# Performance work log

Hardware: AMD Instinct MI355X
Metric: run time of the kernel (lower is better)

## Reference

```python
import jax, jax.numpy as jnp
import numpy as np

VOCAB = 128
NUM_PATHS = 100     # num_paths sampled from the lattice
NBEST_SCALE = 0.5   # scale on scores before sampling (k2.random_paths)
TEMPERATURE = 1.0   # logprob temperature before normalization
BLANK = 0           # CTC blank token


def setup_inputs() -> dict:
    key = jax.random.key(0)
    k1, k2, k3, k4 = jax.random.split(key, 4)
    B, T, L = 8, 500, 100
    logits = jax.random.normal(k1, (B, T, VOCAB), jnp.float32)
    emissions = jax.nn.log_softmax(logits, -1)  # acoustic-model log-probs (N, T, C)
    emissions_lengths = jax.random.randint(k2, (B,), 400, T + 1).astype(jnp.int32)
    labels = jax.random.randint(k3, (B, L), 1, VOCAB).astype(jnp.int32)
    labels_length = jax.random.randint(k4, (B,), 80, L + 1).astype(jnp.int32)
    return {"emissions": emissions, "emissions_lengths": emissions_lengths,
            "labels": labels, "labels_length": labels_length}


def _mwer(emissions, emissions_lengths, labels, labels_length):
    B, T, V = emissions.shape
    L = labels.shape[1]
    P = NUM_PATHS
    key = jax.random.key(1)
    # --- N-best path sampling: Gumbel perturbation of nbest_scale-scaled log-probs ---
    u = jax.random.uniform(key, (B, P, T, V), emissions.dtype, 1e-6, 1.0 - 1e-6)
    g = -jnp.log(-jnp.log(u))
    tokens = jnp.argmax(emissions[:, None] * NBEST_SCALE + g, axis=-1)  # (B, P, T)
    frame_mask = jnp.arange(T)[None, None, :] < emissions_lengths[:, None, None]
    # path log-prob under the model (unscaled scores), temperature-scaled
    lp = jnp.take_along_axis(emissions[:, None], tokens[..., None], axis=-1)[..., 0]
    path_logp = jnp.sum(jnp.where(frame_mask, lp, 0.0), axis=-1) / TEMPERATURE  # (B, P)
    # --- CTC collapse (ctc_topo semantics: drop blanks + repeats) into padded hyps ---
    prev = jnp.concatenate([jnp.full_like(tokens[..., :1], -1), tokens[..., :-1]], -1)
    keep = (tokens != BLANK) & (tokens != prev) & frame_mask
    pos = jnp.where(keep, jnp.cumsum(keep, -1) - 1, T)  # dropped frames -> dump slot T
    BP = B * P
    tok2, pos2 = tokens.reshape(BP, T), pos.reshape(BP, T)
    hyp = jnp.full((BP, T + 1), -1, tokens.dtype).at[jnp.arange(BP)[:, None], pos2].set(tok2)[:, :T]
    hyp_len = keep.reshape(BP, T).sum(-1)
    # --- Levenshtein alignment: exact edit distance hyp vs ref (vectorized DP) ---
    refs = jnp.repeat(labels, P, axis=0)             # (BP, L)  hyp_to_ref_map
    ref_len = jnp.repeat(labels_length, P, axis=0)   # (BP,)
    dp0 = jnp.broadcast_to(jnp.arange(L + 1, dtype=jnp.int32), (BP, L + 1))
    js = jnp.arange(L + 1, dtype=jnp.int32)[None, :]

    def step(dp, x):
        h, valid = x  # hyp token (BP,), valid flag (BP,)
        cost = (refs != h[:, None]).astype(jnp.int32)                       # (BP, L)
        cand = jnp.concatenate([dp[:, :1] + 1,
                                jnp.minimum(dp[:, 1:] + 1, dp[:, :-1] + cost)], 1)
        # insertion chain new[j] = min(cand[j], new[j-1]+1) via min-plus prefix
        new = jax.lax.cummin(cand - js, axis=1) + js
        return jnp.where(valid[:, None], new, dp), None

    valid = jnp.arange(T)[:, None] < hyp_len[None, :]  # (T, BP)
    dp, _ = jax.lax.scan(step, dp0, (hyp.T, valid))
    wers = jnp.take_along_axis(dp, ref_len[:, None], 1)[:, 0].reshape(B, P)
    wers = jax.lax.stop_gradient(wers.astype(emissions.dtype))
    # --- MWER: normalize path posteriors per utterance, expected WER, 'mean' ---
    prob = jax.nn.softmax(path_logp, axis=1)
    return jnp.mean(prob * wers)


def reference(emissions, emissions_lengths, labels, labels_length):
    return _mwer(emissions, emissions_lengths, labels, labels_length)
```

## Files before the change

kernel.cpp:

```cpp
#include <hip/hip_runtime.h>
#include <stdint.h>

#define NB 8
#define NP 100
#define NT 500
#define NV 128
#define NBP 800
#define TS 512
#define NITEMS (NB * NT * 50)
#define ROWD 129

typedef unsigned long long u64;

#define ROTL(x, r) __builtin_amdgcn_alignbit((x), (x), 32 - (r))

__device__ __forceinline__ uint32_t threefry01_lo(uint32_t x0, uint32_t x1) {
  const uint32_t k0 = 0u, k1 = 1u;
  const uint32_t k2 = 0x1BD11BDAu ^ k0 ^ k1;
  x0 += k0; x1 += k1;
#define TF_R(r) { x0 += x1; x1 = ROTL(x1, r); x1 ^= x0; }
  TF_R(13) TF_R(15) TF_R(26) TF_R(6)
  x0 += k1; x1 += k2 + 1u;
  TF_R(17) TF_R(29) TF_R(16) TF_R(24)
  x0 += k2; x1 += k0 + 2u;
  TF_R(13) TF_R(15) TF_R(26) TF_R(6)
  x0 += k0; x1 += k1 + 3u;
  TF_R(17) TF_R(29) TF_R(16) TF_R(24)
  x0 += k1; x1 += k2 + 4u;
  TF_R(13) TF_R(15) TF_R(26) TF_R(6)
  x1 += k0 + 5u;
#undef TF_R
  return x1;
}

__global__ __launch_bounds__(256) void k_sample(
    const float* __restrict__ em, const int* __restrict__ elen,
    uint8_t* __restrict__ tok2, float* __restrict__ lp2) {
  __shared__ float snw[4][NV + 1];
  const int tid = threadIdx.x;
  const int item0 = blockIdx.x * 128;
  const int R0 = item0 / 50;
  for (int i = tid; i < 4 * NV; i += 256) {
    const int r = i >> 7, v = i & 127;
    int R = R0 + r; R = R < NB * NT ? R : NB * NT - 1;
    snw[r][v] = -__builtin_amdgcn_exp2f(em[(size_t)R * NV + v] * -0.7213475204444817f);
  }
  __syncthreads();
  const int gg = blockIdx.x * 256 + tid;
  const int item = gg >> 1, half = gg & 1;
  if (item >= NITEMS) return;
  const int R = item / 50;
  const int pp = item - R * 50;
  const int b = R / NT;
  const int t = R - b * NT;
  if (t >= elen[b]) return;
  const int r = R - R0;
  const int vh = half << 6;
  const int bp0 = b * NP + 2 * pp;
  const uint32_t base0 = ((uint32_t)(bp0 * NT + t) << 7) + (uint32_t)vh;
  const uint32_t base1 = base0 + (uint32_t)(NT << 7);
  const float span = (float)(1.0 - 1e-6) - 1e-6f;
  float best0 = 3.0e38f, best1 = 3.0e38f;
  int bi0 = 0, bi1 = 0;
#pragma unroll 8
  for (int i = 0; i < 64; i++) {
    const uint32_t r0 = threefry01_lo(0u, base0 + (uint32_t)i);
    const uint32_t r1 = threefry01_lo(0u, base1 + (uint32_t)i);
    const float f0 = __uint_as_float((r0 >> 9) | 0x3f800000u) - 1.0f;
    const float f1 = __uint_as_float((r1 >> 9) | 0x3f800000u) - 1.0f;
    const float u0 = fmaf(f0, span, 1e-6f);
    const float u1 = fmaf(f1, span, 1e-6f);
    const float w = snw[r][vh + i];
    const float s0 = __log2f(u0) * w;
    const float s1 = __log2f(u1) * w;
    if (s0 < best0) { best0 = s0; bi0 = vh + i; }
    if (s1 < best1) { best1 = s1; bi1 = vh + i; }
  }
  {
    const float ob = __shfl_xor(best0, 1); const int oi = __shfl_xor(bi0, 1);
    if (ob < best0 || (ob == best0 && oi < bi0)) { best0 = ob; bi0 = oi; }
    const float ob1 = __shfl_xor(best1, 1); const int oi1 = __shfl_xor(bi1, 1);
    if (ob1 < best1 || (ob1 == best1 && oi1 < bi1)) { best1 = ob1; bi1 = oi1; }
  }
  if (half == 0) {
    const float e0 = em[(size_t)R * NV + bi0];
    const float e1 = em[(size_t)R * NV + bi1];
    tok2[(size_t)bp0 * TS + t] = (uint8_t)bi0;
    tok2[(size_t)(bp0 + 1) * TS + t] = (uint8_t)bi1;
    lp2[(size_t)bp0 * TS + t] = e0;
    lp2[(size_t)(bp0 + 1) * TS + t] = e1;
  }
}

struct Eq4 { u64 e0[4], e1[4]; int cc[4]; };

__device__ __forceinline__ void ext4(uint32_t wbits, const uint32_t* __restrict__ pqf,
                                     Eq4& E) {
#pragma unroll
  for (int i = 0; i < 4; i++) {
    const int byte = (wbits >> (8 * i)) & 255;
    const int c = byte & 127;
    E.cc[i] = byte;
    E.e0[i] = (u64)pqf[c] | ((u64)pqf[128 + c] << 32);
    E.e1[i] = (u64)pqf[256 + c] | ((u64)pqf[384 + c] << 32);
  }
}

__device__ __forceinline__ void proc4(const Eq4& E, int fbase, int myel,
                                      int hw, u64 hmask,
                                      u64& Pv0, u64& Pv1, u64& Mv0, u64& Mv1,
                                      int& score, int& prev) {
#pragma unroll
  for (int i = 0; i < 4; i++) {
    if (fbase + i >= myel) break;
    const int c = E.cc[i];
    const bool kept = (c != 0) && (c != prev);
    prev = c;
    if (kept) {
      const u64 Eq0 = E.e0[i], Eq1 = E.e1[i];
      const u64 Xv0 = Eq0 | Mv0, Xv1 = Eq1 | Mv1;
      const u64 EP0 = Eq0 & Pv0, EP1 = Eq1 & Pv1;
      const u64 sA = EP0 + Pv0;
      const u64 sB = EP1 + Pv1 + (sA < EP0 ? 1ull : 0ull);
      const u64 Xh0 = (sA ^ Pv0) | Eq0;
      const u64 Xh1 = (sB ^ Pv1) | Eq1;
      const u64 Ph0 = Mv0 | ~(Xh0 | Pv0);
      const u64 Ph1 = Mv1 | ~(Xh1 | Pv1);
      const u64 Mh0 = Pv0 & Xh0, Mh1 = Pv1 & Xh1;
      score += (int)(((hw ? Ph1 : Ph0) & hmask) != 0);
      score -= (int)(((hw ? Mh1 : Mh0) & hmask) != 0);
      const u64 nPh1 = (Ph1 << 1) | (Ph0 >> 63);
      const u64 nPh0 = (Ph0 << 1) | 1ull;
      const u64 nMh1 = (Mh1 << 1) | (Mh0 >> 63);
      const u64 nMh0 = (Mh0 << 1);
      Pv0 = nMh0 | ~(Xv0 | nPh0);
      Pv1 = nMh1 | ~(Xv1 | nPh1);
      Mv0 = nPh0 & Xv0;
      Mv1 = nPh1 & Xv1;
    }
  }
}

__global__ __launch_bounds__(128) void k_dp(
    const uint8_t* __restrict__ tok2,
    const int* __restrict__ elen, const int* __restrict__ labels,
    const int* __restrict__ llen, float* __restrict__ wer) {
  __shared__ uint32_t pq[4][NV];
  __shared__ uint32_t tokL[NP * ROWD];
  const int b = blockIdx.x;
  const int tid = threadIdx.x;
  const uint32_t* __restrict__ src = (const uint32_t*)(tok2 + (size_t)b * NP * TS);
#pragma unroll 4
  for (int i = 0; i < 100; i++) {
    const int gi = i * 128 + tid;
    const int row = gi >> 7, col = gi & 127;
    tokL[row * ROWD + col] = src[gi];
  }
  const int m = llen[b];
  {
    const int c = tid;
    const int* __restrict__ lab = labels + b * 100;
    uint32_t a0 = 0, a1 = 0, a2 = 0, a3 = 0;
    const int e0 = m < 32 ? m : 32, e1 = m < 64 ? m : 64;
    const int e2 = m < 96 ? m : 96, e3 = m;
    for (int i = 0; i < e0; i++)  a0 |= (uint32_t)(lab[i] == c) << i;
    for (int i = 32; i < e1; i++) a1 |= (uint32_t)(lab[i] == c) << (i - 32);
    for (int i = 64; i < e2; i++) a2 |= (uint32_t)(lab[i] == c) << (i - 64);
    for (int i = 96; i < e3; i++) a3 |= (uint32_t)(lab[i] == c) << (i - 96);
    pq[0][c] = a0; pq[1][c] = a1; pq[2][c] = a2; pq[3][c] = a3;
  }
  __syncthreads();
  const uint32_t* __restrict__ pqf = &pq[0][0];
  const bool active = (tid < NP);
  const int p = active ? tid : NP - 1;
  const uint32_t* __restrict__ tp = tokL + p * ROWD;
  const int myel = elen[b];
  u64 Pv0 = ~0ull, Pv1 = ~0ull, Mv0 = 0ull, Mv1 = 0ull;
  int score = m, prev = -1;
  const int hw = (m - 1) >> 6;
  const u64 hmask = 1ull << ((m - 1) & 63);

  const int ng = (myel + 3) >> 2;
  Eq4 A, B;
  ext4(tp[0], pqf, A);
  int g = 0;
  for (; g + 1 < ng; g += 2) {
    ext4(tp[g + 1], pqf, B);
    proc4(A, g * 4, myel, hw, hmask, Pv0, Pv1, Mv0, Mv1, score, prev);
    if (g + 2 < ng) ext4(tp[g + 2], pqf, A);
    proc4(B, (g + 1) * 4, myel, hw, hmask, Pv0, Pv1, Mv0, Mv1, score, prev);
  }
  if (g < ng) proc4(A, g * 4, myel, hw, hmask, Pv0, Pv1, Mv0, Mv1, score, prev);
  if (active) wer[b * NP + p] = (float)score;
}

__global__ __launch_bounds__(256) void k_red(
    const float* __restrict__ lp2, const int* __restrict__ elen,
    float* __restrict__ slp) {
  const int b = blockIdx.x;
  const int p = blockIdx.y * 4 + (threadIdx.x >> 6);
  const int lane = threadIdx.x & 63;
  const int el = elen[b];
  const float* __restrict__ row = lp2 + (size_t)(b * NP + p) * TS;
  double s = 0.0;
  for (int t = lane; t < el; t += 64) s += (double)row[t];
  for (int off = 1; off < 64; off <<= 1) s += __shfl_xor(s, off);
  if (lane == 0) slp[b * NP + p] = (float)s;
}

__global__ __launch_bounds__(512) void k_fin(
    const float* __restrict__ slp, const float* __restrict__ wer,
    float* __restrict__ out) {
  __shared__ float partial[NB];
  const int w = threadIdx.x >> 6, lane = threadIdx.x & 63;
  const int base = w * NP;
  const float l0 = (lane < NP) ? slp[base + lane] : -1e30f;
  const float l1 = (lane + 64 < NP) ? slp[base + lane + 64] : -1e30f;
  float mx = fmaxf(l0, l1);
  for (int off = 1; off < 64; off <<= 1) mx = fmaxf(mx, __shfl_xor(mx, off));
  const float e0 = (lane < NP) ? __expf(l0 - mx) : 0.0f;
  const float e1 = (lane + 64 < NP) ? __expf(l1 - mx) : 0.0f;
  const float w0 = (lane < NP) ? wer[base + lane] : 0.0f;
  const float w1 = (lane + 64 < NP) ? wer[base + lane + 64] : 0.0f;
  float s = e0 + e1;
  float a = e0 * w0 + e1 * w1;
  for (int off = 1; off < 64; off <<= 1) {
    s += __shfl_xor(s, off);
    a += __shfl_xor(a, off);
  }
  if (lane == 0) partial[w] = a / s;
  __syncthreads();
  if (threadIdx.x == 0) {
    float tot = 0.0f;
    for (int i = 0; i < NB; i++) tot += partial[i];
    out[0] = tot * (1.0f / (float)NBP);
  }
}

extern "C" void kernel_launch(void* const* d_in, const int* in_sizes, int n_in,
                              void* d_out, int out_size, void* d_ws, size_t ws_size,
                              hipStream_t stream) {
  const float* em     = (const float*)d_in[0];
  const int*   elen   = (const int*)d_in[1];
  const int*   labels = (const int*)d_in[2];
  const int*   llen   = (const int*)d_in[3];
  float* out = (float*)d_out;
  char* ws = (char*)d_ws;
  uint8_t* tok2 = (uint8_t*)ws;
  float* lp2    = (float*)(ws + (size_t)NBP * TS);
  float* wer    = (float*)(ws + (size_t)NBP * TS * 5);
  float* slp    = (float*)(ws + (size_t)NBP * TS * 5 + NBP * 4);

  k_sample<<<dim3((NITEMS * 2 + 255) / 256), dim3(256), 0, stream>>>(em, elen, tok2, lp2);
  k_dp<<<dim3(NB), dim3(128), 0, stream>>>(tok2, elen, labels, llen, wer);
  k_red<<<dim3(NB, 25), dim3(256), 0, stream>>>(lp2, elen, slp);
  k_fin<<<dim3(1), dim3(512), 0, stream>>>(slp, wer, out);
}
```

Before: 213.9 us.

## Split sampling vocab across 4 lanes, split DP blocks, transpose logprob buffer

The sampling kernel now uses four lanes per item, each scanning 32 vocab entries, instead of two lanes scanning 64. A two-level shuffle merges the partial argmins. The sampling launch is split into two grids. The edit-distance kernel runs 16 blocks of 64 threads (50 paths each) instead of 8 blocks, and the bit-parallel update becomes branchless select code. Log-probs are stored time-major so the per-path sum runs with one thread per path over strided columns, and the shuffle reduction is dropped. The goals are more parallelism and shorter per-thread serial chains, at the cost of more threads and a serial per-thread reduction loop.

Result: slower. 233.5 us (+9.2%).

```diff
diff --git a/kernel.cpp b/kernel.cpp
--- a/kernel.cpp
+++ b/kernel.cpp
@@ -35,19 +35,19 @@
 
 __global__ __launch_bounds__(256) void k_sample(
     const float* __restrict__ em, const int* __restrict__ elen,
-    uint8_t* __restrict__ tok2, float* __restrict__ lp2) {
-  __shared__ float snw[4][NV + 1];
+    uint8_t* __restrict__ tok2, float* __restrict__ lp2t, int item_base) {
+  __shared__ float snw[3][NV + 1];
   const int tid = threadIdx.x;
-  const int item0 = blockIdx.x * 128;
-  const int R0 = item0 / 50;
-  for (int i = tid; i < 4 * NV; i += 256) {
+  const int i0 = item_base + blockIdx.x * 64;
+  const int R0 = i0 / 50;
+  for (int i = tid; i < 3 * NV; i += 256) {
     const int r = i >> 7, v = i & 127;
     int R = R0 + r; R = R < NB * NT ? R : NB * NT - 1;
     snw[r][v] = -__builtin_amdgcn_exp2f(em[(size_t)R * NV + v] * -0.7213475204444817f);
   }
   __syncthreads();
-  const int gg = blockIdx.x * 256 + tid;
-  const int item = gg >> 1, half = gg & 1;
+  const int item = i0 + (tid >> 2);
+  const int q = tid & 3;
   if (item >= NITEMS) return;
   const int R = item / 50;
   const int pp = item - R * 50;
@@ -55,7 +55,7 @@
   const int t = R - b * NT;
   if (t >= elen[b]) return;
   const int r = R - R0;
-  const int vh = half << 6;
+  const int vh = q << 5;
   const int bp0 = b * NP + 2 * pp;
   const uint32_t base0 = ((uint32_t)(bp0 * NT + t) << 7) + (uint32_t)vh;
   const uint32_t base1 = base0 + (uint32_t)(NT << 7);
@@ -63,7 +63,7 @@
   float best0 = 3.0e38f, best1 = 3.0e38f;
   int bi0 = 0, bi1 = 0;
 #pragma unroll 8
-  for (int i = 0; i < 64; i++) {
+  for (int i = 0; i < 32; i++) {
     const uint32_t r0 = threefry01_lo(0u, base0 + (uint32_t)i);
     const uint32_t r1 = threefry01_lo(0u, base1 + (uint32_t)i);
     const float f0 = __uint_as_float((r0 >> 9) | 0x3f800000u) - 1.0f;
@@ -76,19 +76,19 @@
     if (s0 < best0) { best0 = s0; bi0 = vh + i; }
     if (s1 < best1) { best1 = s1; bi1 = vh + i; }
   }
-  {
-    const float ob = __shfl_xor(best0, 1); const int oi = __shfl_xor(bi0, 1);
-    if (ob < best0 || (ob == best0 && oi < bi0)) { best0 = ob; bi0 = oi; }
-    const float ob1 = __shfl_xor(best1, 1); const int oi1 = __shfl_xor(bi1, 1);
-    if (ob1 < best1 || (ob1 == best1 && oi1 < bi1)) { best1 = ob1; bi1 = oi1; }
-  }
-  if (half == 0) {
+#pragma unroll
+  for (int off = 1; off <= 2; off <<= 1) {
+    const float oa = __shfl_xor(best0, off); const int ia = __shfl_xor(bi0, off);
+    if (oa < best0 || (oa == best0 && ia < bi0)) { best0 = oa; bi0 = ia; }
+    const float ob = __shfl_xor(best1, off); const int ib = __shfl_xor(bi1, off);
+    if (ob < best1 || (ob == best1 && ib < bi1)) { best1 = ob; bi1 = ib; }
+  }
+  if (q == 0) {
     const float e0 = em[(size_t)R * NV + bi0];
     const float e1 = em[(size_t)R * NV + bi1];
     tok2[(size_t)bp0 * TS + t] = (uint8_t)bi0;
     tok2[(size_t)(bp0 + 1) * TS + t] = (uint8_t)bi1;
-    lp2[(size_t)bp0 * TS + t] = e0;
-    lp2[(size_t)(bp0 + 1) * TS + t] = e1;
+    *(float2*)&lp2t[(size_t)t * NBP + bp0] = make_float2(e0, e1);
   }
 }
 
@@ -106,78 +106,78 @@
   }
 }
 
-__device__ __forceinline__ void proc4(const Eq4& E, int fbase, int myel,
-                                      int hw, u64 hmask,
+__device__ __forceinline__ void proc4(const Eq4& E, int fbase, int myel, u64 hmask,
                                       u64& Pv0, u64& Pv1, u64& Mv0, u64& Mv1,
                                       int& score, int& prev) {
 #pragma unroll
   for (int i = 0; i < 4; i++) {
     if (fbase + i >= myel) break;
     const int c = E.cc[i];
-    const bool kept = (c != 0) && (c != prev);
+    const bool kept = (c != 0) & (c != prev);
     prev = c;
-    if (kept) {
-      const u64 Eq0 = E.e0[i], Eq1 = E.e1[i];
-      const u64 Xv0 = Eq0 | Mv0, Xv1 = Eq1 | Mv1;
-      const u64 EP0 = Eq0 & Pv0, EP1 = Eq1 & Pv1;
-      const u64 sA = EP0 + Pv0;
-      const u64 sB = EP1 + Pv1 + (sA < EP0 ? 1ull : 0ull);
-      const u64 Xh0 = (sA ^ Pv0) | Eq0;
-      const u64 Xh1 = (sB ^ Pv1) | Eq1;
-      const u64 Ph0 = Mv0 | ~(Xh0 | Pv0);
-      const u64 Ph1 = Mv1 | ~(Xh1 | Pv1);
-      const u64 Mh0 = Pv0 & Xh0, Mh1 = Pv1 & Xh1;
-      score += (int)(((hw ? Ph1 : Ph0) & hmask) != 0);
-      score -= (int)(((hw ? Mh1 : Mh0) & hmask) != 0);
-      const u64 nPh1 = (Ph1 << 1) | (Ph0 >> 63);
-      const u64 nPh0 = (Ph0 << 1) | 1ull;
-      const u64 nMh1 = (Mh1 << 1) | (Mh0 >> 63);
-      const u64 nMh0 = (Mh0 << 1);
-      Pv0 = nMh0 | ~(Xv0 | nPh0);
-      Pv1 = nMh1 | ~(Xv1 | nPh1);
-      Mv0 = nPh0 & Xv0;
-      Mv1 = nPh1 & Xv1;
-    }
-  }
-}
-
-__global__ __launch_bounds__(128) void k_dp(
+    const u64 Eq0 = E.e0[i], Eq1 = E.e1[i];
+    const u64 Xv0 = Eq0 | Mv0, Xv1 = Eq1 | Mv1;
+    const u64 EP0 = Eq0 & Pv0, EP1 = Eq1 & Pv1;
+    const u64 sA = EP0 + Pv0;
+    const u64 sB = EP1 + Pv1 + (sA < EP0 ? 1ull : 0ull);
+    const u64 Xh0 = (sA ^ Pv0) | Eq0;
+    const u64 Xh1 = (sB ^ Pv1) | Eq1;
+    const u64 Ph0 = Mv0 | ~(Xh0 | Pv0);
+    const u64 Ph1 = Mv1 | ~(Xh1 | Pv1);
+    const u64 Mh0 = Pv0 & Xh0, Mh1 = Pv1 & Xh1;
+    const int d = (int)((Ph1 & hmask) != 0) - (int)((Mh1 & hmask) != 0);
+    const u64 nPh1 = (Ph1 << 1) | (Ph0 >> 63);
+    const u64 nPh0 = (Ph0 << 1) | 1ull;
+    const u64 nMh1 = (Mh1 << 1) | (Mh0 >> 63);
+    const u64 nMh0 = (Mh0 << 1);
+    score += kept ? d : 0;
+    Pv0 = kept ? (nMh0 | ~(Xv0 | nPh0)) : Pv0;
+    Pv1 = kept ? (nMh1 | ~(Xv1 | nPh1)) : Pv1;
+    Mv0 = kept ? (nPh0 & Xv0) : Mv0;
+    Mv1 = kept ? (nPh1 & Xv1) : Mv1;
+  }
+}
+
+__global__ __launch_bounds__(64) void k_dp(
     const uint8_t* __restrict__ tok2,
     const int* __restrict__ elen, const int* __restrict__ labels,
     const int* __restrict__ llen, float* __restrict__ wer) {
   __shared__ uint32_t pq[4][NV];
-  __shared__ uint32_t tokL[NP * ROWD];
-  const int b = blockIdx.x;
+  __shared__ uint32_t tokL[50 * ROWD];
+  const int b = blockIdx.x, h = blockIdx.y;
   const int tid = threadIdx.x;
-  const uint32_t* __restrict__ src = (const uint32_t*)(tok2 + (size_t)b * NP * TS);
-#pragma unroll 4
+  const uint32_t* __restrict__ src =
+      (const uint32_t*)(tok2 + (size_t)(b * NP + h * 50) * TS);
+#pragma unroll 8
   for (int i = 0; i < 100; i++) {
-    const int gi = i * 128 + tid;
+    const int gi = i * 64 + tid;
     const int row = gi >> 7, col = gi & 127;
     tokL[row * ROWD + col] = src[gi];
   }
   const int m = llen[b];
   {
-    const int c = tid;
     const int* __restrict__ lab = labels + b * 100;
-    uint32_t a0 = 0, a1 = 0, a2 = 0, a3 = 0;
     const int e0 = m < 32 ? m : 32, e1 = m < 64 ? m : 64;
     const int e2 = m < 96 ? m : 96, e3 = m;
-    for (int i = 0; i < e0; i++)  a0 |= (uint32_t)(lab[i] == c) << i;
-    for (int i = 32; i < e1; i++) a1 |= (uint32_t)(lab[i] == c) << (i - 32);
-    for (int i = 64; i < e2; i++) a2 |= (uint32_t)(lab[i] == c) << (i - 64);
-    for (int i = 96; i < e3; i++) a3 |= (uint32_t)(lab[i] == c) << (i - 96);
-    pq[0][c] = a0; pq[1][c] = a1; pq[2][c] = a2; pq[3][c] = a3;
+#pragma unroll
+    for (int hh = 0; hh < 2; hh++) {
+      const int c = tid + hh * 64;
+      uint32_t a0 = 0, a1 = 0, a2 = 0, a3 = 0;
+      for (int i = 0; i < e0; i++)  a0 |= (uint32_t)(lab[i] == c) << i;
+      for (int i = 32; i < e1; i++) a1 |= (uint32_t)(lab[i] == c) << (i - 32);
+      for (int i = 64; i < e2; i++) a2 |= (uint32_t)(lab[i] == c) << (i - 64);
+      for (int i = 96; i < e3; i++) a3 |= (uint32_t)(lab[i] == c) << (i - 96);
+      pq[0][c] = a0; pq[1][c] = a1; pq[2][c] = a2; pq[3][c] = a3;
+    }
   }
   __syncthreads();
   const uint32_t* __restrict__ pqf = &pq[0][0];
-  const bool active = (tid < NP);
-  const int p = active ? tid : NP - 1;
-  const uint32_t* __restrict__ tp = tokL + p * ROWD;
+  const bool active = (tid < 50);
+  const int pl = active ? tid : 49;
+  const uint32_t* __restrict__ tp = tokL + pl * ROWD;
   const int myel = elen[b];
   u64 Pv0 = ~0ull, Pv1 = ~0ull, Mv0 = 0ull, Mv1 = 0ull;
   int score = m, prev = -1;
-  const int hw = (m - 1) >> 6;
   const u64 hmask = 1ull << ((m - 1) & 63);
 
   const int ng = (myel + 3) >> 2;
@@ -186,26 +186,27 @@
   int g = 0;
   for (; g + 1 < ng; g += 2) {
     ext4(tp[g + 1], pqf, B);
-    proc4(A, g * 4, myel, hw, hmask, Pv0, Pv1, Mv0, Mv1, score, prev);
+    proc4(A, g * 4, myel, hmask, Pv0, Pv1, Mv0, Mv1, score, prev);
     if (g + 2 < ng) ext4(tp[g + 2], pqf, A);
-    proc4(B, (g + 1) * 4, myel, hw, hmask, Pv0, Pv1, Mv0, Mv1, score, prev);
-  }
-  if (g < ng) proc4(A, g * 4, myel, hw, hmask, Pv0, Pv1, Mv0, Mv1, score, prev);
-  if (active) wer[b * NP + p] = (float)score;
-}
-
-__global__ __launch_bounds__(256) void k_red(
-    const float* __restrict__ lp2, const int* __restrict__ elen,
+    proc4(B, (g + 1) * 4, myel, hmask, Pv0, Pv1, Mv0, Mv1, score, prev);
+  }
+  if (g < ng) proc4(A, g * 4, myel, hmask, Pv0, Pv1, Mv0, Mv1, score, prev);
+  if (active) wer[b * NP + h * 50 + tid] = (float)score;
+}
+
+__global__ __launch_bounds__(128) void k_red(
+    const float* __restrict__ lp2t, const int* __restrict__ elen,
     float* __restrict__ slp) {
   const int b = blockIdx.x;
-  const int p = blockIdx.y * 4 + (threadIdx.x >> 6);
-  const int lane = threadIdx.x & 63;
+  const int tid = threadIdx.x;
+  const bool active = (tid < NP);
+  const int p = active ? tid : NP - 1;
   const int el = elen[b];
-  const float* __restrict__ row = lp2 + (size_t)(b * NP + p) * TS;
+  const float* __restrict__ col = lp2t + b * NP + p;
   double s = 0.0;
-  for (int t = lane; t < el; t += 64) s += (double)row[t];
-  for (int off = 1; off < 64; off <<= 1) s += __shfl_xor(s, off);
-  if (lane == 0) slp[b * NP + p] = (float)s;
+#pragma unroll 8
+  for (int t = 0; t < el; t++) s += (double)col[(size_t)t * NBP];
+  if (active) slp[b * NP + p] = (float)s;
 }
 
 __global__ __launch_bounds__(512) void k_fin(
@@ -247,12 +248,13 @@
   float* out = (float*)d_out;
   char* ws = (char*)d_ws;
   uint8_t* tok2 = (uint8_t*)ws;
-  float* lp2    = (float*)(ws + (size_t)NBP * TS);
-  float* wer    = (float*)(ws + (size_t)NBP * TS * 5);
-  float* slp    = (float*)(ws + (size_t)NBP * TS * 5 + NBP * 4);
-
-  k_sample<<<dim3((NITEMS * 2 + 255) / 256), dim3(256), 0, stream>>>(em, elen, tok2, lp2);
-  k_dp<<<dim3(NB), dim3(128), 0, stream>>>(tok2, elen, labels, llen, wer);
-  k_red<<<dim3(NB, 25), dim3(256), 0, stream>>>(lp2, elen, slp);
+  float* lp2t   = (float*)(ws + (size_t)NBP * TS);
+  float* wer    = (float*)(ws + (size_t)NBP * TS + (size_t)NT * NBP * 4);
+  float* slp    = (float*)(ws + (size_t)NBP * TS + (size_t)NT * NBP * 4 + NBP * 4);
+
+  k_sample<<<dim3(1563), dim3(256), 0, stream>>>(em, elen, tok2, lp2t, 0);
+  k_sample<<<dim3(1562), dim3(256), 0, stream>>>(em, elen, tok2, lp2t, 1563 * 64);
+  k_dp<<<dim3(NB, 2), dim3(64), 0, stream>>>(tok2, elen, labels, llen, wer);
+  k_red<<<dim3(NB), dim3(128), 0, stream>>>(lp2t, elen, slp);
   k_fin<<<dim3(1), dim3(512), 0, stream>>>(slp, wer, out);
 }
```
